# Optimization experiments

Hardware: AMD Instinct MI355X
Metric: run time of the kernel (lower is better)

The kernel has to match this reference:

```python
import jax, jax.numpy as jnp
import numpy as np

EPS = 1e-5


def setup_inputs() -> dict:
    key = jax.random.key(0)
    ks = jax.random.split(key, 6)
    B, N, F = 8, 8192, 64
    xyzs = jax.random.uniform(ks[0], (B, N, 3), dtype=jnp.float32)
    feats = jax.random.normal(ks[1], (B, N, F), dtype=jnp.float32)
    c_in = 3 + F  # 67
    dims = [(64, c_in), (64, 64), (128, 64)]
    inp = {"xyzs": xyzs, "feats": feats}
    for i, (co, ci) in enumerate(dims, start=1):
        inp[f"w{i}"] = jax.random.normal(ks[1 + i], (co, ci), dtype=jnp.float32) / np.sqrt(ci)
        inp[f"b{i}"] = jnp.zeros((co,), jnp.float32)
        inp[f"g{i}"] = jnp.ones((co,), jnp.float32)
        inp[f"bt{i}"] = jnp.zeros((co,), jnp.float32)
        inp[f"m{i}"] = jnp.zeros((co,), jnp.float32)
        inp[f"v{i}"] = jnp.ones((co,), jnp.float32)
    return inp


def sample_farthest_points(xyz, S):
    # Iterative FPS starting from index 0 (pytorch3d default random_start_point=False).
    B, N, _ = xyz.shape
    barange = jnp.arange(B)

    def step(carry, _):
        mind, last = carry                      # mind: [B,N] min sq-dist to selected set
        lastp = xyz[barange, last]              # [B,3]
        d = jnp.sum((xyz - lastp[:, None, :]) ** 2, -1)
        mind = jnp.minimum(mind, d)
        nxt = jnp.argmax(mind, axis=1).astype(jnp.int32)
        return (mind, nxt), nxt

    init = (jnp.full((B, N), 1e10, xyz.dtype), jnp.zeros((B,), jnp.int32))
    _, rest = jax.lax.scan(step, init, None, length=S - 1)  # [S-1, B]
    idx = jnp.concatenate([jnp.zeros((1, B), jnp.int32), rest], 0).T  # [B,S]
    return xyz[barange[:, None], idx], idx


def ball_query(centers, xyz, K, radius):
    # First-K-in-radius semantics of pytorch3d.ops.ball_query; pad idx with -1,
    # pad gathered points with zeros (masked_gather behavior).
    B, N, _ = xyz.shape
    d2 = (jnp.sum(centers ** 2, -1)[:, :, None]
          + jnp.sum(xyz ** 2, -1)[:, None, :]
          - 2.0 * jnp.einsum('bsd,bnd->bsn', centers, xyz))  # [B,S,N]
    within = d2 <= radius * radius
    skey = jnp.where(within, jnp.arange(N, dtype=jnp.int32), N)
    negvals, idx = jax.lax.top_k(-skey, K)      # K smallest keys = first K in-radius
    valid = (-negvals) < N                       # [B,S,K]
    group_idx = jnp.where(valid, idx, -1)
    gathered = xyz[jnp.arange(B)[:, None, None], jnp.where(valid, idx, 0)]  # [B,S,K,3]
    group_xyz = jnp.where(valid[..., None], gathered, 0.0)
    return group_idx, group_xyz


def _mlp_layer(x, w, b, g, bt, m, v):
    # 1x1 Conv2d over channel axis + BatchNorm (eval stats) + ReLU; x: [B,S,K,Cin]
    y = jnp.einsum('bskc,oc->bsko', x, w) + b
    y = g * (y - m) * jax.lax.rsqrt(v + EPS) + bt
    return jax.nn.relu(y)


def reference(xyzs, feats, w1, b1, g1, bt1, m1, v1,
              w2, b2, g2, bt2, m2, v2, w3, b3, g3, bt3, m3, v3):
    S, K, radius = 2048, 32, 0.2
    B = xyzs.shape[0]
    center_xyzs, _ = sample_farthest_points(xyzs, S)             # [B,S,3]
    group_idxs, group_xyzs = ball_query(center_xyzs, xyzs, K, radius)
    group_xyzs = group_xyzs - center_xyzs[:, :, None, :]          # relative coords
    batch_idxs = jnp.arange(B)[:, None, None]
    gf = feats[batch_idxs, jnp.where(group_idxs < 0, 0, group_idxs)]  # [B,S,K,F]
    gf = jnp.concatenate([group_xyzs, gf], axis=-1)
    gf = gf * (group_idxs != -1)[..., None].astype(gf.dtype)      # zero padded slots
    x = _mlp_layer(gf, w1, b1, g1, bt1, m1, v1)
    x = _mlp_layer(x, w2, b2, g2, bt2, m2, v2)
    x = _mlp_layer(x, w3, b3, g3, bt3, m3, v3)
    center_feats = jnp.max(x, axis=2)                             # max over neighbors
    return center_xyzs, center_feats
```

## Files before the change

### kernel.cpp

```cpp
#include <hip/hip_runtime.h>


#define NPTS 8192
#define SCTR 2048
#define NB   8
#define KNN  32
#define NF   64
#define WT_FLOATS (67*64 + 64*64 + 64*128)
#define PROG_STRIDE 32

typedef float v2f __attribute__((ext_vector_type(2)));

__device__ __forceinline__ v2f fps_sqdist_v2(v2f px, v2f py, v2f pz,
                                             v2f lx, v2f ly, v2f lz) {
#pragma clang fp contract(off)
  v2f dx = px - lx;
  v2f dy = py - ly;
  v2f dz = pz - lz;
  v2f xx = dx * dx;
  v2f yy = dy * dy;
  v2f zz = dz * dz;
  return (xx + yy) + zz;
}

__device__ __forceinline__ float sumsq3(float x, float y, float z) {
#pragma clang fp contract(off)
  return (x * x + y * y) + z * z;
}

__device__ __forceinline__ float bq_d2(float sc, float sx,
                                       float cx, float cy, float cz,
                                       float x, float y, float z) {
#pragma clang fp contract(off)
  float dt = fmaf(cz, z, fmaf(cy, y, cx * x));
  return (sc + sx) - 2.0f * dt;
}

template <int CTRL>
__device__ __forceinline__ unsigned long long kmax_dpp(unsigned long long k) {
  int lo = (int)(unsigned int)(k & 0xFFFFFFFFull);
  int hi = (int)(unsigned int)(k >> 32);
  int slo = __builtin_amdgcn_update_dpp(lo, lo, CTRL, 0xF, 0xF, false);
  int shi = __builtin_amdgcn_update_dpp(hi, hi, CTRL, 0xF, 0xF, false);
  unsigned long long sk =
      ((unsigned long long)(unsigned int)shi << 32) | (unsigned int)slo;
  return sk > k ? sk : k;
}

__global__ __launch_bounds__(256) void init_kernel(
    const float* __restrict__ w1, const float* __restrict__ w2,
    const float* __restrict__ w3, float* __restrict__ wT,
    int* __restrict__ prog)
{
  const int t = threadIdx.x;
  if (blockIdx.x == 0) prog[t] = 0;
  int idx = blockIdx.x * 256 + t;
  if (idx < 67*64) {
    int c = idx >> 6, o = idx & 63;
    wT[idx] = w1[o*67 + c];
  } else if (idx < 67*64 + 64*64) {
    int r = idx - 67*64; int c = r >> 6, o = r & 63;
    wT[idx] = w2[o*64 + c];
  } else if (idx < 67*64 + 64*64 + 64*128) {
    int r = idx - (67*64 + 64*64); int c = r >> 7, o = r & 127;
    wT[idx] = w3[o*64 + c];
  }
}

__global__ __launch_bounds__(256, 1) void mega_kernel(
    const float* __restrict__ xyzs, const float* __restrict__ feats,
    float* centers, const float* __restrict__ wT, int* prog,
    const float* __restrict__ b1, const float* __restrict__ g1, const float* __restrict__ bt1,
    const float* __restrict__ m1, const float* __restrict__ v1,
    const float* __restrict__ b2, const float* __restrict__ g2, const float* __restrict__ bt2,
    const float* __restrict__ m2, const float* __restrict__ v2,
    const float* __restrict__ b3, const float* __restrict__ g3, const float* __restrict__ bt3,
    const float* __restrict__ m3, const float* __restrict__ v3,
    float* out_feats)
{
  __shared__ __align__(16) float smem[26640];

  if (blockIdx.x < NB) {
    __builtin_amdgcn_s_setprio(3);
    const int b = blockIdx.x;
    const int t = threadIdx.x;
    const float* xb = xyzs + (size_t)b * NPTS * 3;
    int* prog_b = prog + b * PROG_STRIDE;
    float* cb_ = centers + (size_t)b * SCTR * 3;

    float* sX = smem;
    float* sY = smem + 8192;
    float* sZ = smem + 16384;
    int*  hist = (int*)(smem + 24576);
    unsigned long long* redk = (unsigned long long*)(smem + 26624);

    for (int i = t; i < NPTS; i += 256) {
      sX[i] = xb[3*i+0];
      sY[i] = xb[3*i+1];
      sZ[i] = xb[3*i+2];
    }
    if (t == 0) hist[0] = 0;
    __syncthreads();

    const int t4 = 4 * t;

    const float4 xA = *(const float4*)(sX + 0    + t4);
    const float4 yA = *(const float4*)(sY + 0    + t4);
    const float4 zA = *(const float4*)(sZ + 0    + t4);
    const float4 xB = *(const float4*)(sX + 1024 + t4);
    const float4 yB = *(const float4*)(sY + 1024 + t4);
    const float4 zB = *(const float4*)(sZ + 1024 + t4);
    const float4 xC = *(const float4*)(sX + 2048 + t4);
    const float4 yC = *(const float4*)(sY + 2048 + t4);
    const float4 zC = *(const float4*)(sZ + 2048 + t4);
    const float4 xD = *(const float4*)(sX + 3072 + t4);
    const float4 yD = *(const float4*)(sY + 3072 + t4);
    const float4 zD = *(const float4*)(sZ + 3072 + t4);
    const float4 xE = *(const float4*)(sX + 4096 + t4);
    const float4 yE = *(const float4*)(sY + 4096 + t4);
    const float4 zE = *(const float4*)(sZ + 4096 + t4);
    const float4 xF = *(const float4*)(sX + 5120 + t4);
    const float4 yF = *(const float4*)(sY + 5120 + t4);
    const float4 zF = *(const float4*)(sZ + 5120 + t4);
    const float4 xG = *(const float4*)(sX + 6144 + t4);
    const float4 yG = *(const float4*)(sY + 6144 + t4);
    const float4 zG = *(const float4*)(sZ + 6144 + t4);
    const float4 xH = *(const float4*)(sX + 7168 + t4);
    const float4 yH = *(const float4*)(sY + 7168 + t4);
    const float4 zH = *(const float4*)(sZ + 7168 + t4);

    float4 mA = make_float4(1e10f,1e10f,1e10f,1e10f);
    float4 mB = mA, mC = mA, mD = mA, mE = mA, mF = mA, mG = mA, mH = mA;

    float lx = sX[0], ly = sY[0], lz = sZ[0];

#define FPS_QUAD(QX, QY, QZ, MV, QOFF, BV, BG)                                  \
  do {                                                                          \
    v2f d;                                                                      \
    d = fps_sqdist_v2((v2f){QX.x,QX.y}, (v2f){QY.x,QY.y}, (v2f){QZ.x,QZ.y},     \
                      lxv, lyv, lzv);                                           \
    MV.x = fminf(MV.x, d.x); if (MV.x > BV) { BV = MV.x; BG = (QOFF)+t4+0; }    \
    MV.y = fminf(MV.y, d.y); if (MV.y > BV) { BV = MV.y; BG = (QOFF)+t4+1; }    \
    d = fps_sqdist_v2((v2f){QX.z,QX.w}, (v2f){QY.z,QY.w}, (v2f){QZ.z,QZ.w},     \
                      lxv, lyv, lzv);                                           \
    MV.z = fminf(MV.z, d.x); if (MV.z > BV) { BV = MV.z; BG = (QOFF)+t4+2; }    \
    MV.w = fminf(MV.w, d.y); if (MV.w > BV) { BV = MV.w; BG = (QOFF)+t4+3; }    \
  } while (0)

    for (int s = 1; s < SCTR; ++s) {
      float bv0 = -1.0f, bv1 = -1.0f; int bg0 = 0, bg1 = 0;
      {
        v2f lxv = {lx, lx}, lyv = {ly, ly}, lzv = {lz, lz};
        FPS_QUAD(xA, yA, zA, mA, 0,    bv0, bg0);
        FPS_QUAD(xB, yB, zB, mB, 1024, bv0, bg0);
        FPS_QUAD(xC, yC, zC, mC, 2048, bv0, bg0);
        FPS_QUAD(xD, yD, zD, mD, 3072, bv0, bg0);
        FPS_QUAD(xE, yE, zE, mE, 4096, bv1, bg1);
        FPS_QUAD(xF, yF, zF, mF, 5120, bv1, bg1);
        FPS_QUAD(xG, yG, zG, mG, 6144, bv1, bg1);
        FPS_QUAD(xH, yH, zH, mH, 7168, bv1, bg1);
      }
      float bv = bv0; int bg = bg0;
      if (bv1 > bv0) { bv = bv1; bg = bg1; }

      unsigned long long key =
          ((unsigned long long)__float_as_uint(bv) << 13) |
          (unsigned long long)(8191 - bg);

      key = kmax_dpp<0x111>(key);
      key = kmax_dpp<0x112>(key);
      key = kmax_dpp<0x114>(key);
      key = kmax_dpp<0x118>(key);
      key = kmax_dpp<0x142>(key);
      key = kmax_dpp<0x143>(key);

      int pb = s & 1;
      if ((t & 63) == 63) redk[pb*4 + (t >> 6)] = key;
      __syncthreads();

      unsigned long long k4 = redk[pb*4 + (t & 3)];
      k4 = kmax_dpp<0xB1>(k4);
      k4 = kmax_dpp<0x4E>(k4);

      int i0 = 8191 - (int)(k4 & 0x1FFFull);
      lx = sX[i0]; ly = sY[i0]; lz = sZ[i0];
      if (t == 0) hist[s] = i0;

      if ((s & 31) == 31) {
        if (t < 32) {
          int ci  = (s - 31) + t;
          int idx = hist[ci];
          float x = sX[idx], y = sY[idx], z = sZ[idx];
          float* o = cb_ + 3*ci;
          o[0] = x; o[1] = y; o[2] = z;
        }
        if (t == 0)
          __hip_atomic_store(prog_b, s - 31, __ATOMIC_RELEASE, __HIP_MEMORY_SCOPE_AGENT);
      }
    }
#undef FPS_QUAD
    __builtin_amdgcn_s_sleep(127);
    if (t == 0)
      __hip_atomic_store(prog_b, SCTR, __ATOMIC_RELEASE, __HIP_MEMORY_SCOPE_AGENT);
    return;
  }

  constexpr float R2 = (float)(0.2 * 0.2);
  const int t    = threadIdx.x;
  const int jb   = blockIdx.x - NB;
  const int half = t >> 7;
  const int ht   = t & 127;
  const int w    = ht >> 6;
  const int lane = ht & 63;
  const int cid  = 2 * jb + half;
  const int b    = cid & 7;
  const int s    = cid >> 3;
  const int bid  = b * SCTR + s;
  const float* xb = xyzs + (size_t)b * NPTS * 3;

  float* in_  = smem + half * 4352;
  float* y_   = in_ + 2176;
  int*   gidx = (int*)(smem + 8704) + half * KNN;
  float* csl  = smem + 8768 + half * 4;

  if (ht == 0) {
    int* pb_ = prog + b * PROG_STRIDE;
    while (__hip_atomic_load(pb_, __ATOMIC_ACQUIRE, __HIP_MEMORY_SCOPE_AGENT) <= s)
      __builtin_amdgcn_s_sleep(64);
    const float* cg = centers + (size_t)bid * 3;
    csl[0] = cg[0]; csl[1] = cg[1]; csl[2] = cg[2];
  }
  __syncthreads();
  const float cx = csl[0], cy = csl[1], cz = csl[2];
  const float sc = sumsq3(cx, cy, cz);

  int cnt = 0;
  for (int base = 0; base < NPTS && cnt < KNN; base += 64) {
    int n = base + lane;
    float x = xb[n*3+0], y = xb[n*3+1], z = xb[n*3+2];
    float sx = sumsq3(x, y, z);
    float d2 = bq_d2(sc, sx, cx, cy, cz, x, y, z);
    bool within = (d2 <= R2);
    unsigned long long mk = __ballot(within);
    int rank = __popcll(mk & ((1ull << lane) - 1ull));
    int slot = cnt + rank;
    if (within && slot < KNN) gidx[slot] = n;
    cnt += (int)__popcll(mk);
  }
  if (cnt > KNN) cnt = KNN;
  __syncthreads();

#pragma unroll 4
  for (int k2 = 0; k2 < 16; ++k2) {
    int k = 2*k2 + w;
    int gk = (k < cnt) ? gidx[k] : -1;
    float fv = 0.f, xv = 0.f;
    if (gk >= 0) {
      fv = feats[((size_t)b * NPTS + gk) * NF + lane];
      if (lane < 3) xv = xb[gk*3 + lane] - csl[lane];
    }
    in_[k*68 + 3 + lane] = fv;
    if (lane < 3) in_[k*68 + lane] = xv;
    if (lane == 3) in_[k*68 + 67] = 0.f;
  }
  __syncthreads();

  const int g  = lane >> 3;
  const int h  = lane & 7;
  const int ob = w*32 + 4*h;
  const float* w1T = wT;
  const float* w2T = wT + 67*64;
  const float* w3T = wT + 67*64 + 64*64;

#define FMA_COL(AS0, AS1, AS2, AS3, WV)                                      \
  do {                                                                       \
    acc[0][0]=fmaf(AS0, WV.x, acc[0][0]); acc[0][1]=fmaf(AS0, WV.y, acc[0][1]); \
    acc[0][2]=fmaf(AS0, WV.z, acc[0][2]); acc[0][3]=fmaf(AS0, WV.w, acc[0][3]); \
    acc[1][0]=fmaf(AS1, WV.x, acc[1][0]); acc[1][1]=fmaf(AS1, WV.y, acc[1][1]); \
    acc[1][2]=fmaf(AS1, WV.z, acc[1][2]); acc[1][3]=fmaf(AS1, WV.w, acc[1][3]); \
    acc[2][0]=fmaf(AS2, WV.x, acc[2][0]); acc[2][1]=fmaf(AS2, WV.y, acc[2][1]); \
    acc[2][2]=fmaf(AS2, WV.z, acc[2][2]); acc[2][3]=fmaf(AS2, WV.w, acc[2][3]); \
    acc[3][0]=fmaf(AS3, WV.x, acc[3][0]); acc[3][1]=fmaf(AS3, WV.y, acc[3][1]); \
    acc[3][2]=fmaf(AS3, WV.z, acc[3][2]); acc[3][3]=fmaf(AS3, WV.w, acc[3][3]); \
  } while (0)

#define MLP_CHUNK(SRC, WBASE, WSTRIDE, WOFF)                                 \
  do {                                                                       \
    float4 a0 = *(const float4*)((SRC) + (4*g+0)*68 + c0);                   \
    float4 a1 = *(const float4*)((SRC) + (4*g+1)*68 + c0);                   \
    float4 a2 = *(const float4*)((SRC) + (4*g+2)*68 + c0);                   \
    float4 a3 = *(const float4*)((SRC) + (4*g+3)*68 + c0);                   \
    float4 wv0 = *(const float4*)(WBASE + (c0+0)*(WSTRIDE) + (WOFF));        \
    float4 wv1 = *(const float4*)(WBASE + (c0+1)*(WSTRIDE) + (WOFF));        \
    float4 wv2 = *(const float4*)(WBASE + (c0+2)*(WSTRIDE) + (WOFF));        \
    float4 wv3 = *(const float4*)(WBASE + (c0+3)*(WSTRIDE) + (WOFF));        \
    FMA_COL(a0.x, a1.x, a2.x, a3.x, wv0);                                    \
    FMA_COL(a0.y, a1.y, a2.y, a3.y, wv1);                                    \
    FMA_COL(a0.z, a1.z, a2.z, a3.z, wv2);                                    \
    FMA_COL(a0.w, a1.w, a2.w, a3.w, wv3);                                    \
  } while (0)

  {
    float acc[4][4];
#pragma unroll
    for (int i=0;i<4;++i)
#pragma unroll
      for (int j=0;j<4;++j) acc[i][j]=0.f;
#pragma unroll 2
    for (int c0 = 0; c0 < 68; c0 += 4) {
      MLP_CHUNK(in_, w1T, 64, ob);
    }
    float scl[4], shf[4];
#pragma unroll
    for (int j=0;j<4;++j) {
      int o = ob + j;
      float r = g1[o] * rsqrtf(v1[o] + 1e-5f);
      scl[j] = r;
      shf[j] = (b1[o] - m1[o]) * r + bt1[o];
    }
#pragma unroll
    for (int i=0;i<4;++i) {
      float4 out;
      out.x = fmaxf(fmaf(acc[i][0], scl[0], shf[0]), 0.f);
      out.y = fmaxf(fmaf(acc[i][1], scl[1], shf[1]), 0.f);
      out.z = fmaxf(fmaf(acc[i][2], scl[2], shf[2]), 0.f);
      out.w = fmaxf(fmaf(acc[i][3], scl[3], shf[3]), 0.f);
      *(float4*)(y_ + (4*g+i)*68 + ob) = out;
    }
  }
  __syncthreads();

  {
    float acc[4][4];
#pragma unroll
    for (int i=0;i<4;++i)
#pragma unroll
      for (int j=0;j<4;++j) acc[i][j]=0.f;
#pragma unroll 2
    for (int c0 = 0; c0 < 64; c0 += 4) {
      MLP_CHUNK(y_, w2T, 64, ob);
    }
    float scl[4], shf[4];
#pragma unroll
    for (int j=0;j<4;++j) {
      int o = ob + j;
      float r = g2[o] * rsqrtf(v2[o] + 1e-5f);
      scl[j] = r;
      shf[j] = (b2[o] - m2[o]) * r + bt2[o];
    }
    __syncthreads();
#pragma unroll
    for (int i=0;i<4;++i) {
      float4 out;
      out.x = fmaxf(fmaf(acc[i][0], scl[0], shf[0]), 0.f);
      out.y = fmaxf(fmaf(acc[i][1], scl[1], shf[1]), 0.f);
      out.z = fmaxf(fmaf(acc[i][2], scl[2], shf[2]), 0.f);
      out.w = fmaxf(fmaf(acc[i][3], scl[3], shf[3]), 0.f);
      *(float4*)(in_ + (4*g+i)*68 + ob) = out;
    }
  }
  __syncthreads();

  for (int p = 0; p < 2; ++p) {
    const int o3 = w*64 + p*32 + 4*h;
    float acc[4][4];
#pragma unroll
    for (int i=0;i<4;++i)
#pragma unroll
      for (int j=0;j<4;++j) acc[i][j]=0.f;
#pragma unroll 2
    for (int c0 = 0; c0 < 64; c0 += 4) {
      MLP_CHUNK(in_, w3T, 128, o3);
    }
    float scl[4], shf[4];
#pragma unroll
    for (int j=0;j<4;++j) {
      int o = o3 + j;
      float r = g3[o] * rsqrtf(v3[o] + 1e-5f);
      scl[j] = r;
      shf[j] = (b3[o] - m3[o]) * r + bt3[o];
    }
    float vm[4];
#pragma unroll
    for (int j=0;j<4;++j) {
      float q0 = fmaxf(fmaf(acc[0][j], scl[j], shf[j]), 0.f);
      float q1 = fmaxf(fmaf(acc[1][j], scl[j], shf[j]), 0.f);
      float q2 = fmaxf(fmaf(acc[2][j], scl[j], shf[j]), 0.f);
      float q3 = fmaxf(fmaf(acc[3][j], scl[j], shf[j]), 0.f);
      vm[j] = fmaxf(fmaxf(q0,q1), fmaxf(q2,q3));
    }
#pragma unroll
    for (int mk = 8; mk < 64; mk <<= 1) {
#pragma unroll
      for (int j=0;j<4;++j) vm[j] = fmaxf(vm[j], __shfl_xor(vm[j], mk));
    }
    if (g == 0) {
      float* dst = out_feats + (size_t)bid*128 + o3;
      *(float4*)dst = make_float4(vm[0], vm[1], vm[2], vm[3]);
    }
  }
#undef MLP_CHUNK
#undef FMA_COL
}

extern "C" void kernel_launch(void* const* d_in, const int* in_sizes, int n_in,
                              void* d_out, int out_size, void* d_ws, size_t ws_size,
                              hipStream_t stream) {
  const float* xyzs  = (const float*)d_in[0];
  const float* feats = (const float*)d_in[1];
  const float* w1  = (const float*)d_in[2];
  const float* b1  = (const float*)d_in[3];
  const float* g1  = (const float*)d_in[4];
  const float* bt1 = (const float*)d_in[5];
  const float* m1  = (const float*)d_in[6];
  const float* v1  = (const float*)d_in[7];
  const float* w2  = (const float*)d_in[8];
  const float* b2  = (const float*)d_in[9];
  const float* g2  = (const float*)d_in[10];
  const float* bt2 = (const float*)d_in[11];
  const float* m2  = (const float*)d_in[12];
  const float* v2  = (const float*)d_in[13];
  const float* w3  = (const float*)d_in[14];
  const float* b3  = (const float*)d_in[15];
  const float* g3  = (const float*)d_in[16];
  const float* bt3 = (const float*)d_in[17];
  const float* m3  = (const float*)d_in[18];
  const float* v3  = (const float*)d_in[19];

  float* out       = (float*)d_out;
  float* centers   = out;
  float* out_feats = out + (size_t)NB * SCTR * 3;
  float* wT        = (float*)d_ws;
  int*   prog      = (int*)((float*)d_ws + WT_FLOATS);

  hipLaunchKernelGGL(init_kernel, dim3(65), dim3(256), 0, stream,
                     w1, w2, w3, wT, prog);
  hipLaunchKernelGGL(mega_kernel, dim3(NB + NB * SCTR / 2), dim3(256), 0, stream,
                     xyzs, feats, centers, wT, prog,
                     b1, g1, bt1, m1, v1,
                     b2, g2, bt2, m2, v2,
                     b3, g3, bt3, m3, v3,
                     out_feats);
}
```

Before: 2.030 ms.

## Publish FPS indices through a flagged per-center ring instead of a progress counter

The FPS blocks now write each selected point index into a per-center ring slot, tagged with a high-bit valid flag, every 16 steps using relaxed atomics. Previously they wrote center coordinates and a release-ordered progress counter every 32 steps. Consumer blocks spin on their own slot and read the center coordinates straight from the input points. The full center output is written once after FPS finishes. This removes global stores and release fences from the serial FPS loop and lets grouping blocks start sooner, at the cost of a larger ring in the workspace that must be zeroed each call.

```diff
diff --git a/kernel.cpp b/kernel.cpp
--- a/kernel.cpp
+++ b/kernel.cpp
@@ -7,7 +7,7 @@
 #define KNN  32
 #define NF   64
 #define WT_FLOATS (67*64 + 64*64 + 64*128)
-#define PROG_STRIDE 32
+#define RING_U32  (NB * SCTR)
 
 typedef float v2f __attribute__((ext_vector_type(2)));
 
@@ -50,11 +50,11 @@
 __global__ __launch_bounds__(256) void init_kernel(
     const float* __restrict__ w1, const float* __restrict__ w2,
     const float* __restrict__ w3, float* __restrict__ wT,
-    int* __restrict__ prog)
+    unsigned* __restrict__ ring)
 {
   const int t = threadIdx.x;
-  if (blockIdx.x == 0) prog[t] = 0;
   int idx = blockIdx.x * 256 + t;
+  if (idx < RING_U32) ring[idx] = 0u;
   if (idx < 67*64) {
     int c = idx >> 6, o = idx & 63;
     wT[idx] = w1[o*67 + c];
@@ -69,7 +69,7 @@
 
 __global__ __launch_bounds__(256, 1) void mega_kernel(
     const float* __restrict__ xyzs, const float* __restrict__ feats,
-    float* centers, const float* __restrict__ wT, int* prog,
+    float* centers, const float* __restrict__ wT, unsigned* ring,
     const float* __restrict__ b1, const float* __restrict__ g1, const float* __restrict__ bt1,
     const float* __restrict__ m1, const float* __restrict__ v1,
     const float* __restrict__ b2, const float* __restrict__ g2, const float* __restrict__ bt2,
@@ -85,7 +85,7 @@
     const int b = blockIdx.x;
     const int t = threadIdx.x;
     const float* xb = xyzs + (size_t)b * NPTS * 3;
-    int* prog_b = prog + b * PROG_STRIDE;
+    unsigned* ring_b = ring + b * SCTR;
     float* cb_ = centers + (size_t)b * SCTR * 3;
 
     float* sX = smem;
@@ -133,6 +133,7 @@
     float4 mB = mA, mC = mA, mD = mA, mE = mA, mF = mA, mG = mA, mH = mA;
 
     float lx = sX[0], ly = sY[0], lz = sZ[0];
+    int stash = 0;
 
 #define FPS_QUAD(QX, QY, QZ, MV, QOFF, BV, BG)                                  \
   do {                                                                          \
@@ -186,22 +187,21 @@
       lx = sX[i0]; ly = sY[i0]; lz = sZ[i0];
       if (t == 0) hist[s] = i0;
 
-      if ((s & 31) == 31) {
-        if (t < 32) {
-          int ci  = (s - 31) + t;
-          int idx = hist[ci];
-          float x = sX[idx], y = sY[idx], z = sZ[idx];
-          float* o = cb_ + 3*ci;
-          o[0] = x; o[1] = y; o[2] = z;
-        }
-        if (t == 0)
-          __hip_atomic_store(prog_b, s - 31, __ATOMIC_RELEASE, __HIP_MEMORY_SCOPE_AGENT);
+      if (t < 16 && (s & 15) == t) stash = i0;
+      if ((s & 15) == 15 && t < 16) {
+        __hip_atomic_store(ring_b + (s - 15) + t,
+                           0x80000000u | (unsigned)stash,
+                           __ATOMIC_RELAXED, __HIP_MEMORY_SCOPE_AGENT);
       }
     }
 #undef FPS_QUAD
-    __builtin_amdgcn_s_sleep(127);
-    if (t == 0)
-      __hip_atomic_store(prog_b, SCTR, __ATOMIC_RELEASE, __HIP_MEMORY_SCOPE_AGENT);
+
+    __syncthreads();
+    for (int ss = t; ss < SCTR; ss += 256) {
+      int i = hist[ss];
+      float* o = cb_ + 3 * ss;
+      o[0] = sX[i]; o[1] = sY[i]; o[2] = sZ[i];
+    }
     return;
   }
 
@@ -224,10 +224,16 @@
   float* csl  = smem + 8768 + half * 4;
 
   if (ht == 0) {
-    int* pb_ = prog + b * PROG_STRIDE;
-    while (__hip_atomic_load(pb_, __ATOMIC_ACQUIRE, __HIP_MEMORY_SCOPE_AGENT) <= s)
-      __builtin_amdgcn_s_sleep(64);
-    const float* cg = centers + (size_t)bid * 3;
+    int i0 = 0;
+    if (s > 0) {
+      const unsigned* rp = ring + b * SCTR + s;
+      unsigned v;
+      while (!((v = __hip_atomic_load(rp, __ATOMIC_RELAXED,
+                                      __HIP_MEMORY_SCOPE_AGENT)) & 0x80000000u))
+        __builtin_amdgcn_s_sleep(32);
+      i0 = (int)(v & 0x1FFFu);
+    }
+    const float* cg = xb + 3 * i0;
     csl[0] = cg[0]; csl[1] = cg[1]; csl[2] = cg[2];
   }
   __syncthreads();
@@ -431,12 +437,12 @@
   float* centers   = out;
   float* out_feats = out + (size_t)NB * SCTR * 3;
   float* wT        = (float*)d_ws;
-  int*   prog      = (int*)((float*)d_ws + WT_FLOATS);
+  unsigned* ring   = (unsigned*)((float*)d_ws + WT_FLOATS);
 
   hipLaunchKernelGGL(init_kernel, dim3(65), dim3(256), 0, stream,
-                     w1, w2, w3, wT, prog);
+                     w1, w2, w3, wT, ring);
   hipLaunchKernelGGL(mega_kernel, dim3(NB + NB * SCTR / 2), dim3(256), 0, stream,
-                     xyzs, feats, centers, wT, prog,
+                     xyzs, feats, centers, wT, ring,
                      b1, g1, bt1, m1, v1,
                      b2, g2, bt2, m2, v2,
                      b3, g3, bt3, m3, v3,
```

Measured after the change: 2.032 ms. No clear change (+0.1%).
